# Kernel tuning notes

Hardware: AMD Instinct MI355X
Metric: run time of the kernel (lower is better)

The kernel has to match this reference:

```python
import jax, jax.numpy as jnp
import numpy as np
from functools import partial

L, B, E, H, NL = 512, 16, 768, 12, 12
D = E // H  # head dim = 64
FF = 4 * E
LN_EPS = 1e-5


def gelu_new(x):
    # HF openai-gpt ACT_FNS['gelu'] (tanh approximation)
    c = np.sqrt(2.0 / np.pi).astype(np.float32)
    return 0.5 * x * (1.0 + jnp.tanh(c * (x + 0.044715 * x * x * x)))


def layer_norm(x, g, b):
    mu = jnp.mean(x, axis=-1, keepdims=True)
    var = jnp.mean(jnp.square(x - mu), axis=-1, keepdims=True)
    return (x - mu) * jax.lax.rsqrt(var + LN_EPS) * g + b


def setup_inputs() -> dict:
    key = jax.random.key(0)
    ks = jax.random.split(key, 8)
    s = 0.02
    x = jax.random.normal(ks[0], (L, B, E), dtype=jnp.float32)
    custom_mask = jnp.ones((B, L), dtype=jnp.float32)
    pos_emb = s * jax.random.normal(ks[1], (L, E), dtype=jnp.float32)
    # stacked per-layer params (leading axis = layer)
    params = {
        'c_attn_w': s * jax.random.normal(ks[2], (NL, E, 3 * E), dtype=jnp.float32),
        'c_attn_b': jnp.zeros((NL, 3 * E), dtype=jnp.float32),
        'attn_proj_w': s * jax.random.normal(ks[3], (NL, E, E), dtype=jnp.float32),
        'attn_proj_b': jnp.zeros((NL, E), dtype=jnp.float32),
        'ln1_g': jnp.ones((NL, E), dtype=jnp.float32),
        'ln1_b': jnp.zeros((NL, E), dtype=jnp.float32),
        'c_fc_w': s * jax.random.normal(ks[4], (NL, E, FF), dtype=jnp.float32),
        'c_fc_b': jnp.zeros((NL, FF), dtype=jnp.float32),
        'mlp_proj_w': s * jax.random.normal(ks[5], (NL, FF, E), dtype=jnp.float32),
        'mlp_proj_b': jnp.zeros((NL, E), dtype=jnp.float32),
        'ln2_g': jnp.ones((NL, E), dtype=jnp.float32),
        'ln2_b': jnp.zeros((NL, E), dtype=jnp.float32),
    }
    return {'x': x, 'custom_mask': custom_mask, 'pos_emb': pos_emb, **params}


def _gpt_forward(x, custom_mask, pos_emb, c_attn_w, c_attn_b, attn_proj_w,
                 attn_proj_b, ln1_g, ln1_b, c_fc_w, c_fc_b, mlp_proj_w,
                 mlp_proj_b, ln2_g, ln2_b):
    Lx, Bx, Ex = x.shape
    h = x.transpose(1, 0, 2) + pos_emb[None, :Lx]  # (B, L, E); dropout = eval identity
    # additive padding mask: (1 - m) * finfo.min, broadcast over heads/queries
    add_mask = (1.0 - custom_mask)[:, None, None, :] * jnp.finfo(jnp.float32).min
    causal = jnp.tril(jnp.ones((Lx, Lx), dtype=jnp.float32))  # bias buffer b

    def block(h, p):
        (caw, cab, apw, apb, g1, b1, fw, fb, pw, pb, g2, b2) = p
        qkv = h @ caw + cab                              # (B, L, 3E)
        q, k, v = jnp.split(qkv, 3, axis=-1)
        q = q.reshape(Bx, Lx, H, D).transpose(0, 2, 1, 3)  # (B, H, L, D)
        k = k.reshape(Bx, Lx, H, D).transpose(0, 2, 1, 3)
        v = v.reshape(Bx, Lx, H, D).transpose(0, 2, 1, 3)
        w = jnp.einsum('bhqd,bhkd->bhqk', q, k) / np.float32(np.sqrt(D))
        w = w * causal + (-10000.0) * (1.0 - causal)     # causal bias masking
        w = w + add_mask
        a = jax.nn.softmax(w, axis=-1)
        o = jnp.einsum('bhqk,bhkd->bhqd', a, v)          # (B, H, L, D)
        o = o.transpose(0, 2, 1, 3).reshape(Bx, Lx, Ex)
        a_out = o @ apw + apb
        n = layer_norm(h + a_out, g1, b1)
        m = gelu_new(n @ fw + fb) @ pw + pb
        h2 = layer_norm(n + m, g2, b2)
        return h2, None

    params = (c_attn_w, c_attn_b, attn_proj_w, attn_proj_b, ln1_g, ln1_b,
              c_fc_w, c_fc_b, mlp_proj_w, mlp_proj_b, ln2_g, ln2_b)
    h, _ = jax.lax.scan(block, h, params)
    return h.transpose(1, 0, 2)  # back to (L, B, E)


def reference(x, custom_mask, pos_emb, c_attn_w, c_attn_b, attn_proj_w,
              attn_proj_b, ln1_g, ln1_b, c_fc_w, c_fc_b, mlp_proj_w,
              mlp_proj_b, ln2_g, ln2_b):
    return _gpt_forward(x, custom_mask, pos_emb, c_attn_w, c_attn_b,
                        attn_proj_w, attn_proj_b, ln1_g, ln1_b, c_fc_w,
                        c_fc_b, mlp_proj_w, mlp_proj_b, ln2_g, ln2_b)
```

## Files before the change

### kernel.cpp

```cpp
#include <hip/hip_runtime.h>
#include <cstdint>
#include <cstddef>


#define LSEQ 512
#define NBATCH 16
#define EDIM 768
#define NHEAD 12
#define NLAYER 12

typedef __attribute__((ext_vector_type(8))) short short8;
typedef __attribute__((ext_vector_type(4))) short short4v;
typedef __attribute__((ext_vector_type(4))) float f32x4;

__device__ __forceinline__ short f2bf(float f) {
  union { float f; unsigned u; } x; x.f = f;
  return (short)((x.u + 0x7FFFu + ((x.u >> 16) & 1u)) >> 16);
}
__device__ __forceinline__ float bf2f(short s) {
  union { unsigned u; float f; } x; x.u = ((unsigned)(unsigned short)s) << 16;
  return x.f;
}

__device__ __forceinline__ void gload_lds16(const void* g, void* l) {
  __builtin_amdgcn_global_load_lds(
      (__attribute__((address_space(1))) void*)(void*)g,
      (__attribute__((address_space(3))) void*)l, 16, 0, 0);
}

__global__ __launch_bounds__(256) void wt_transpose(const float* __restrict__ W,
                                                    short* __restrict__ Wt,
                                                    int K, int N) {
  __shared__ float tile[32][33];
  const int n0 = blockIdx.x * 32, k0 = blockIdx.y * 32;
  const size_t lo = (size_t)blockIdx.z * K * N;
  const float* Ws = W + lo;
  short* Wd = Wt + lo;
  const int tx = threadIdx.x & 31, ty = threadIdx.x >> 5;
#pragma unroll
  for (int i = 0; i < 4; ++i)
    tile[ty + i * 8][tx] = Ws[(size_t)(k0 + ty + i * 8) * N + n0 + tx];
  __syncthreads();
#pragma unroll
  for (int i = 0; i < 4; ++i)
    Wd[(size_t)(n0 + ty + i * 8) * K + k0 + tx] = f2bf(tile[tx][ty + i * 8]);
}

__global__ __launch_bounds__(256) void embed_k(const float* __restrict__ x,
                                               const float* __restrict__ pos,
                                               float* __restrict__ h,
                                               short* __restrict__ hbf) {
  const int row = blockIdx.x;
  const int b = row >> 9, lp = row & 511;
  const int t = threadIdx.x;
#pragma unroll
  for (int i = 0; i < 3; ++i) {
    const int e = t + i * 256;
    float v = x[(size_t)(lp * 16 + b) * 768 + e] + pos[(size_t)lp * 768 + e];
    h[(size_t)row * 768 + e] = v;
    hbf[(size_t)row * 768 + e] = f2bf(v);
  }
}

__global__ __launch_bounds__(256) void final_k(const float* __restrict__ h,
                                               float* __restrict__ out) {
  const int row = blockIdx.x;
  const int lp = row >> 4, b = row & 15;
  const int t = threadIdx.x;
#pragma unroll
  for (int i = 0; i < 3; ++i) {
    const int e = t + i * 256;
    out[(size_t)row * 768 + e] = h[(size_t)(b * 512 + lp) * 768 + e];
  }
}

__global__ __launch_bounds__(256) void ln_fused(const float* __restrict__ A,
                                                const short* __restrict__ B0,
                                                const short* __restrict__ B1,
                                                const float* __restrict__ g,
                                                const float* __restrict__ be,
                                                float* __restrict__ outf,
                                                short* __restrict__ outb) {
  const int row = blockIdx.x * 4 + (threadIdx.x >> 6);
  const int l = threadIdx.x & 63;
  const size_t base = (size_t)row * 768;
  float v[12];
  float s1 = 0.f, s2 = 0.f;
#pragma unroll
  for (int j = 0; j < 3; ++j) {
    const int e = j * 256 + l * 4;
    f32x4 a = *(const f32x4*)&A[base + e];
    short4v b0 = *(const short4v*)&B0[base + e];
    short4v b1 = *(const short4v*)&B1[base + e];
#pragma unroll
    for (int q = 0; q < 4; ++q) {
      float x = a[q] + bf2f(b0[q]) + bf2f(b1[q]);
      v[j * 4 + q] = x; s1 += x; s2 += x * x;
    }
  }
#pragma unroll
  for (int m = 1; m < 64; m <<= 1) {
    s1 += __shfl_xor(s1, m);
    s2 += __shfl_xor(s2, m);
  }
  const float mu = s1 * (1.f / 768.f);
  const float rs = rsqrtf(s2 * (1.f / 768.f) - mu * mu + 1e-5f);
#pragma unroll
  for (int j = 0; j < 3; ++j) {
    const int e = j * 256 + l * 4;
    f32x4 gv = *(const f32x4*)&g[e];
    f32x4 bv = *(const f32x4*)&be[e];
    f32x4 of; short4v ob;
#pragma unroll
    for (int q = 0; q < 4; ++q) {
      float o = (v[j * 4 + q] - mu) * rs * gv[q] + bv[q];
      of[q] = o; ob[q] = f2bf(o);
    }
    *(f32x4*)&outf[base + e] = of;
    *(short4v*)&outb[base + e] = ob;
  }
}

template <int EPI>
__global__ __launch_bounds__(512) void gemm512(const short* __restrict__ A,
                                               const short* __restrict__ Bt,
                                               const float* __restrict__ bias,
                                               short* __restrict__ C,
                                               int N, int K) {
  constexpr int BK = 64;
  __shared__ alignas(16) short Alds[128 * BK];
  __shared__ alignas(16) short Blds[256 * BK];
  const int t = threadIdx.x;
  const int w = t >> 6, l = t & 63;
  const int wr = w >> 2, wc = w & 3;
  const int l15 = l & 15, lhi = l >> 4;
  const int rowA0 = blockIdx.x * 128;
  const int rowB0 = blockIdx.y * 256;

  f32x4 acc[4][4];
#pragma unroll
  for (int mi = 0; mi < 4; ++mi)
#pragma unroll
    for (int ni = 0; ni < 4; ++ni) acc[mi][ni] = (f32x4){0.f, 0.f, 0.f, 0.f};

  const int srl = w * 8 + (l >> 3);
  const int ss = l & 7;

  const short* aptr[2];
#pragma unroll
  for (int i = 0; i < 2; ++i) {
    const int r = i * 64 + srl;
    aptr[i] = A + (size_t)(rowA0 + r) * K + ((ss ^ (r & 7)) << 3);
  }
  const short* bptr[4];
#pragma unroll
  for (int i = 0; i < 4; ++i) {
    const int r = i * 64 + srl;
    bptr[i] = Bt + (size_t)(rowB0 + r) * K + ((ss ^ (r & 7)) << 3);
  }

  for (int kt = 0; kt < K; kt += BK) {
#pragma unroll
    for (int i = 0; i < 2; ++i) {
      gload_lds16(aptr[i], &Alds[(i * 64 + w * 8) * BK]);
      aptr[i] += BK;
    }
#pragma unroll
    for (int i = 0; i < 4; ++i) {
      gload_lds16(bptr[i], &Blds[(i * 64 + w * 8) * BK]);
      bptr[i] += BK;
    }
    __syncthreads();
    short8 af[4][2], bfr[4][2];
#pragma unroll
    for (int mi = 0; mi < 4; ++mi) {
      const int r = wr * 64 + mi * 16 + l15;
#pragma unroll
      for (int kc = 0; kc < 2; ++kc)
        af[mi][kc] = *(const short8*)
            &Alds[r * BK + ((((kc << 2) | lhi) ^ (r & 7)) << 3)];
    }
#pragma unroll
    for (int ni = 0; ni < 4; ++ni) {
      const int r = wc * 64 + ni * 16 + l15;
#pragma unroll
      for (int kc = 0; kc < 2; ++kc)
        bfr[ni][kc] = *(const short8*)
            &Blds[r * BK + ((((kc << 2) | lhi) ^ (r & 7)) << 3)];
    }
#pragma unroll
    for (int mi = 0; mi < 4; ++mi)
#pragma unroll
      for (int ni = 0; ni < 4; ++ni)
#pragma unroll
        for (int kc = 0; kc < 2; ++kc)
          acc[mi][ni] = __builtin_amdgcn_mfma_f32_16x16x32_bf16(
              af[mi][kc], bfr[ni][kc], acc[mi][ni], 0, 0, 0);
    __syncthreads();
  }

  float bv[4];
#pragma unroll
  for (int ni = 0; ni < 4; ++ni) bv[ni] = bias[rowB0 + wc * 64 + ni * 16 + l15];
#pragma unroll
  for (int mi = 0; mi < 4; ++mi) {
#pragma unroll
    for (int ni = 0; ni < 4; ++ni) {
      const int col = rowB0 + wc * 64 + ni * 16 + l15;
#pragma unroll
      for (int i = 0; i < 4; ++i) {
        const int row = rowA0 + wr * 64 + mi * 16 + lhi * 4 + i;
        float v = acc[mi][ni][i] + bv[ni];
        if constexpr (EPI == 1) {
          C[(size_t)row * N + col] = f2bf(v);
        } else {
          float pz = v * fmaf(0.044715f, v * v, 1.0f);
          float e = __expf(-1.5957691216057308f * pz);
          float r = __builtin_amdgcn_rcpf(1.0f + e);
          C[(size_t)row * N + col] = f2bf(v * r);
        }
      }
    }
  }
}

__global__ __launch_bounds__(256) void gemm_pk(const short* __restrict__ A,
                                               const short* __restrict__ Bt,
                                               const float* __restrict__ bias,
                                               short* __restrict__ C,
                                               int N, int Kfull) {
  constexpr int BK = 64;
  __shared__ alignas(16) short Alds[128 * BK];
  __shared__ alignas(16) short Blds[128 * BK];
  const int t = threadIdx.x;
  const int w = t >> 6, l = t & 63;
  const int wr = w >> 1, wc = w & 1;
  const int l15 = l & 15, lhi = l >> 4;
  const int rowA0 = blockIdx.x * 128;
  const int rowB0 = blockIdx.y * 128;
  const int z = blockIdx.z;
  const int Ks = Kfull >> 1;
  const int koff = z * Ks;
  short* Cp = C + (size_t)z * 8192 * N;

  f32x4 acc[4][4];
#pragma unroll
  for (int mi = 0; mi < 4; ++mi)
#pragma unroll
    for (int ni = 0; ni < 4; ++ni) acc[mi][ni] = (f32x4){0.f, 0.f, 0.f, 0.f};

  const int srl = l >> 3;
  const int ss = l & 7;

  const short* aptr[4];
  const short* bptr[4];
#pragma unroll
  for (int i = 0; i < 4; ++i) {
    const int r = i * 32 + w * 8 + srl;
    aptr[i] = A + (size_t)(rowA0 + r) * Kfull + koff + ((ss ^ (r & 7)) << 3);
    bptr[i] = Bt + (size_t)(rowB0 + r) * Kfull + koff + ((ss ^ (r & 7)) << 3);
  }

  for (int kt = 0; kt < Ks; kt += BK) {
#pragma unroll
    for (int i = 0; i < 4; ++i) {
      gload_lds16(aptr[i], &Alds[i * 2048 + w * 512]);
      gload_lds16(bptr[i], &Blds[i * 2048 + w * 512]);
      aptr[i] += BK; bptr[i] += BK;
    }
    __syncthreads();
    short8 af[4][2], bfr[4][2];
#pragma unroll
    for (int mi = 0; mi < 4; ++mi) {
      const int r = wr * 64 + mi * 16 + l15;
#pragma unroll
      for (int kc = 0; kc < 2; ++kc)
        af[mi][kc] = *(const short8*)
            &Alds[r * 64 + ((((kc << 2) | lhi) ^ (r & 7)) << 3)];
    }
#pragma unroll
    for (int ni = 0; ni < 4; ++ni) {
      const int r = wc * 64 + ni * 16 + l15;
#pragma unroll
      for (int kc = 0; kc < 2; ++kc)
        bfr[ni][kc] = *(const short8*)
            &Blds[r * 64 + ((((kc << 2) | lhi) ^ (r & 7)) << 3)];
    }
#pragma unroll
    for (int mi = 0; mi < 4; ++mi)
#pragma unroll
      for (int ni = 0; ni < 4; ++ni)
#pragma unroll
        for (int kc = 0; kc < 2; ++kc)
          acc[mi][ni] = __builtin_amdgcn_mfma_f32_16x16x32_bf16(
              af[mi][kc], bfr[ni][kc], acc[mi][ni], 0, 0, 0);
    __syncthreads();
  }

  float bv[4];
#pragma unroll
  for (int ni = 0; ni < 4; ++ni)
    bv[ni] = (z == 0) ? bias[rowB0 + wc * 64 + ni * 16 + l15] : 0.f;
#pragma unroll
  for (int mi = 0; mi < 4; ++mi) {
#pragma unroll
    for (int ni = 0; ni < 4; ++ni) {
      const int col = rowB0 + wc * 64 + ni * 16 + l15;
#pragma unroll
      for (int i = 0; i < 4; ++i) {
        const int row = rowA0 + wr * 64 + mi * 16 + lhi * 4 + i;
        Cp[(size_t)row * N + col] = f2bf(acc[mi][ni][i] + bv[ni]);
      }
    }
  }
}

__global__ __launch_bounds__(256) void attn_k(const short* __restrict__ qkv,
                                              const float* __restrict__ mask,
                                              short* __restrict__ o) {
  const int qb = blockIdx.x;
  const int hh = blockIdx.y;
  const int b = blockIdx.z;
  const int t = threadIdx.x, w = t >> 6, l = t & 63;
  const int l15 = l & 15, lhi = l >> 4;
  __shared__ alignas(16) short Klds[64 * 64];
  __shared__ alignas(16) short Vlds[64 * 64];
  __shared__ alignas(16) short Plds[4][16 * 72];

  short8 qa[2];
  {
    const size_t base =
        (size_t)(b * LSEQ + qb * 64 + w * 16 + l15) * 2304 + hh * 64;
    qa[0] = *(const short8*)&qkv[base + lhi * 8];
    qa[1] = *(const short8*)&qkv[base + 32 + lhi * 8];
  }
  float mrow[4] = {-1e30f, -1e30f, -1e30f, -1e30f};
  float lrow[4] = {0.f, 0.f, 0.f, 0.f};
  const f32x4 zero4 = {0.f, 0.f, 0.f, 0.f};
  f32x4 oacc[4];
#pragma unroll
  for (int nt = 0; nt < 4; ++nt) oacc[nt] = zero4;

  const int nkt = qb + 1;
  for (int kt = 0; kt < nkt; ++kt) {
    __syncthreads();
    {
      const int kr = t >> 2, cc = (t & 3) * 16;
      const size_t grow = (size_t)(b * LSEQ + kt * 64 + kr) * 2304 + hh * 64;
      short8 k0 = *(const short8*)&qkv[grow + 768 + cc];
      short8 k1 = *(const short8*)&qkv[grow + 768 + cc + 8];
      short8 v0 = *(const short8*)&qkv[grow + 1536 + cc];
      short8 v1 = *(const short8*)&qkv[grow + 1536 + cc + 8];
      const int sw = (kr & 7) << 4;
      *(short8*)((char*)Klds + ((kr * 128 + cc * 2) ^ sw)) = k0;
      *(short8*)((char*)Klds + ((kr * 128 + cc * 2 + 16) ^ sw)) = k1;
#pragma unroll
      for (int e = 0; e < 8; ++e) {
        const int n0 = cc + e, n1 = cc + 8 + e;
        ((short*)Vlds)[((n0 * 128 + kr * 2) ^ ((n0 & 7) << 4)) >> 1] = v0[e];
        ((short*)Vlds)[((n1 * 128 + kr * 2) ^ ((n1 & 7) << 4)) >> 1] = v1[e];
      }
    }
    __syncthreads();

    f32x4 s[4];
#pragma unroll
    for (int jt = 0; jt < 4; ++jt) {
      f32x4 z = zero4;
#pragma unroll
      for (int kc = 0; kc < 2; ++kc) {
        const int rowk = jt * 16 + l15;
        short8 kb = *(const short8*)((char*)Klds +
                     ((rowk * 128 + kc * 64 + lhi * 16) ^ ((rowk & 7) << 4)));
        z = __builtin_amdgcn_mfma_f32_16x16x32_bf16(qa[kc], kb, z, 0, 0, 0);
      }
      s[jt] = z;
    }

    float addm[4];
#pragma unroll
    for (int jt = 0; jt < 4; ++jt)
      addm[jt] = (1.0f - mask[b * LSEQ + kt * 64 + jt * 16 + l15]) *
                 -3.402823466e38f;
#pragma unroll
    for (int jt = 0; jt < 4; ++jt) {
      const int colg = kt * 64 + jt * 16 + l15;
#pragma unroll
      for (int i = 0; i < 4; ++i) {
        const int rowg = qb * 64 + w * 16 + lhi * 4 + i;
        float sv = s[jt][i] * 0.125f;
        if (colg > rowg) sv = -10000.0f;
        s[jt][i] = sv + addm[jt];
      }
    }

    float mnew[4], sc[4];
#pragma unroll
    for (int i = 0; i < 4; ++i) {
      float tm = fmaxf(fmaxf(s[0][i], s[1][i]), fmaxf(s[2][i], s[3][i]));
#pragma unroll
      for (int mm = 1; mm < 16; mm <<= 1) tm = fmaxf(tm, __shfl_xor(tm, mm));
      mnew[i] = fmaxf(mrow[i], tm);
      sc[i] = __expf(mrow[i] - mnew[i]);
      mrow[i] = mnew[i];
    }
#pragma unroll
    for (int i = 0; i < 4; ++i) {
      float ts = 0.f;
#pragma unroll
      for (int jt = 0; jt < 4; ++jt) {
        float p = __expf(s[jt][i] - mnew[i]);
        s[jt][i] = p;
        ts += p;
      }
#pragma unroll
      for (int mm = 1; mm < 16; mm <<= 1) ts += __shfl_xor(ts, mm);
      lrow[i] = lrow[i] * sc[i] + ts;
      oacc[0][i] *= sc[i]; oacc[1][i] *= sc[i];
      oacc[2][i] *= sc[i]; oacc[3][i] *= sc[i];
    }

    short* Pw = &Plds[w][0];
#pragma unroll
    for (int jt = 0; jt < 4; ++jt)
#pragma unroll
      for (int i = 0; i < 4; ++i)
        Pw[(lhi * 4 + i) * 72 + jt * 16 + l15] = f2bf(s[jt][i]);
    __syncthreads();
    short8 pa[2];
#pragma unroll
    for (int kc = 0; kc < 2; ++kc)
      pa[kc] = *(const short8*)&Pw[l15 * 72 + kc * 32 + lhi * 8];

#pragma unroll
    for (int nt = 0; nt < 4; ++nt) {
#pragma unroll
      for (int kc = 0; kc < 2; ++kc) {
        const int rown = nt * 16 + l15;
        short8 vb = *(const short8*)((char*)Vlds +
                     ((rown * 128 + kc * 64 + lhi * 16) ^ ((rown & 7) << 4)));
        oacc[nt] = __builtin_amdgcn_mfma_f32_16x16x32_bf16(pa[kc], vb,
                                                           oacc[nt], 0, 0, 0);
      }
    }
  }

#pragma unroll
  for (int i = 0; i < 4; ++i) {
    const size_t row = (size_t)(b * LSEQ + qb * 64 + w * 16 + lhi * 4 + i);
    const float inv = 1.0f / lrow[i];
#pragma unroll
    for (int nt = 0; nt < 4; ++nt)
      o[row * 768 + hh * 64 + nt * 16 + l15] = f2bf(oacc[nt][i] * inv);
  }
}

extern "C" void kernel_launch(void* const* d_in, const int* in_sizes, int n_in,
                              void* d_out, int out_size, void* d_ws,
                              size_t ws_size, hipStream_t stream) {
  const float* x    = (const float*)d_in[0];
  const float* mask = (const float*)d_in[1];
  const float* pos  = (const float*)d_in[2];
  const float* caw  = (const float*)d_in[3];
  const float* cab  = (const float*)d_in[4];
  const float* apw  = (const float*)d_in[5];
  const float* apb  = (const float*)d_in[6];
  const float* g1   = (const float*)d_in[7];
  const float* b1   = (const float*)d_in[8];
  const float* fw   = (const float*)d_in[9];
  const float* fb   = (const float*)d_in[10];
  const float* pw   = (const float*)d_in[11];
  const float* pb   = (const float*)d_in[12];
  const float* g2   = (const float*)d_in[13];
  const float* b2   = (const float*)d_in[14];

  char* ws = (char*)d_ws;
  size_t off = 0;
  auto alloc = [&](size_t bytes) {
    size_t o = off;
    off += (bytes + 255) & ~(size_t)255;
    return o;
  };
  float* h    = (float*)(ws + alloc(8192ull * 768 * 4));
  short* hbf  = (short*)(ws + alloc(8192ull * 768 * 2));
  float* nrm  = (float*)(ws + alloc(8192ull * 768 * 4));
  short* nbf  = (short*)(ws + alloc(8192ull * 768 * 2));
  short* qkvb = (short*)(ws + alloc(8192ull * 2304 * 2));
  short* obf  = (short*)(ws + alloc(8192ull * 768 * 2));
  short* aout = (short*)(ws + alloc(2ull * 8192 * 768 * 2));
  short* gbf  = (short*)(ws + alloc(8192ull * 3072 * 2));
  short* wt_attn = (short*)(ws + alloc(12ull * 768 * 2304 * 2));
  short* wt_proj = (short*)(ws + alloc(12ull * 768 * 768 * 2));
  short* wt_fc   = (short*)(ws + alloc(12ull * 768 * 3072 * 2));
  short* wt_mlp  = (short*)(ws + alloc(12ull * 3072 * 768 * 2));
  short* aout1 = aout + 8192ull * 768;
  (void)ws_size; (void)in_sizes; (void)n_in; (void)out_size;

  wt_transpose<<<dim3(2304 / 32, 768 / 32, 12), 256, 0, stream>>>(caw, wt_attn, 768, 2304);
  wt_transpose<<<dim3(768 / 32, 768 / 32, 12), 256, 0, stream>>>(apw, wt_proj, 768, 768);
  wt_transpose<<<dim3(3072 / 32, 768 / 32, 12), 256, 0, stream>>>(fw, wt_fc, 768, 3072);
  wt_transpose<<<dim3(768 / 32, 3072 / 32, 12), 256, 0, stream>>>(pw, wt_mlp, 3072, 768);

  embed_k<<<8192, 256, 0, stream>>>(x, pos, h, hbf);

  for (int L = 0; L < 12; ++L) {
    gemm512<1><<<dim3(64, 9), 512, 0, stream>>>(
        hbf, wt_attn + (size_t)L * 2304 * 768, cab + (size_t)L * 2304, qkvb, 2304, 768);
    attn_k<<<dim3(8, 12, 16), 256, 0, stream>>>(qkvb, mask, obf);
    gemm_pk<<<dim3(64, 6, 2), 256, 0, stream>>>(
        obf, wt_proj + (size_t)L * 768 * 768, apb + (size_t)L * 768, aout, 768, 768);
    ln_fused<<<2048, 256, 0, stream>>>(h, aout, aout1, g1 + (size_t)L * 768,
                                       b1 + (size_t)L * 768, nrm, nbf);
    gemm512<2><<<dim3(64, 12), 512, 0, stream>>>(
        nbf, wt_fc + (size_t)L * 768 * 3072, fb + (size_t)L * 3072, gbf, 3072, 768);
    gemm_pk<<<dim3(64, 6, 2), 256, 0, stream>>>(
        gbf, wt_mlp + (size_t)L * 3072 * 768, pb + (size_t)L * 768, aout, 768, 3072);
    ln_fused<<<2048, 256, 0, stream>>>(nrm, aout, aout1, g2 + (size_t)L * 768,
                                       b2 + (size_t)L * 768, h, hbf);
  }

  final_k<<<8192, 256, 0, stream>>>(h, (float*)d_out);
}
```

Before: 3.265 ms.

## Shrink QKV/FC GEMM tiles to 64x256 with 256 threads; fuse final transpose into LN

The QKV and FC GEMMs move from 128x256 tiles with 512 threads (8 waves) to 64x256 tiles with 256 threads (4 waves). This doubles the grid size, which is meant to improve CU occupancy and load balance, at the cost of loading the B tile twice as often per output. Separately, the last layer's LayerNorm now writes directly into the output in (L,B,E) order, which removes the final_k copy kernel and the unused bf16 store.

```diff
diff --git a/kernel.cpp b/kernel.cpp
--- a/kernel.cpp
+++ b/kernel.cpp
@@ -62,18 +62,7 @@
   }
 }
 
-__global__ __launch_bounds__(256) void final_k(const float* __restrict__ h,
-                                               float* __restrict__ out) {
-  const int row = blockIdx.x;
-  const int lp = row >> 4, b = row & 15;
-  const int t = threadIdx.x;
-#pragma unroll
-  for (int i = 0; i < 3; ++i) {
-    const int e = t + i * 256;
-    out[(size_t)row * 768 + e] = h[(size_t)(b * 512 + lp) * 768 + e];
-  }
-}
-
+template <int FINAL>
 __global__ __launch_bounds__(256) void ln_fused(const float* __restrict__ A,
                                                 const short* __restrict__ B0,
                                                 const short* __restrict__ B1,
@@ -105,6 +94,11 @@
   }
   const float mu = s1 * (1.f / 768.f);
   const float rs = rsqrtf(s2 * (1.f / 768.f) - mu * mu + 1e-5f);
+  size_t obase = base;
+  if constexpr (FINAL) {
+    const int b = row >> 9, lp = row & 511;
+    obase = (size_t)(lp * 16 + b) * 768;
+  }
 #pragma unroll
   for (int j = 0; j < 3; ++j) {
     const int e = j * 256 + l * 4;
@@ -116,25 +110,25 @@
       float o = (v[j * 4 + q] - mu) * rs * gv[q] + bv[q];
       of[q] = o; ob[q] = f2bf(o);
     }
-    *(f32x4*)&outf[base + e] = of;
-    *(short4v*)&outb[base + e] = ob;
+    *(f32x4*)&outf[obase + e] = of;
+    if constexpr (!FINAL) *(short4v*)&outb[obase + e] = ob;
   }
 }
 
 template <int EPI>
-__global__ __launch_bounds__(512) void gemm512(const short* __restrict__ A,
+__global__ __launch_bounds__(256) void gemm256(const short* __restrict__ A,
                                                const short* __restrict__ Bt,
                                                const float* __restrict__ bias,
                                                short* __restrict__ C,
                                                int N, int K) {
   constexpr int BK = 64;
-  __shared__ alignas(16) short Alds[128 * BK];
+  __shared__ alignas(16) short Alds[64 * BK];
   __shared__ alignas(16) short Blds[256 * BK];
   const int t = threadIdx.x;
   const int w = t >> 6, l = t & 63;
-  const int wr = w >> 2, wc = w & 3;
+  const int wc = w;
   const int l15 = l & 15, lhi = l >> 4;
-  const int rowA0 = blockIdx.x * 128;
+  const int rowA0 = blockIdx.x * 64;
   const int rowB0 = blockIdx.y * 256;
 
   f32x4 acc[4][4];
@@ -149,32 +143,32 @@
   const short* aptr[2];
 #pragma unroll
   for (int i = 0; i < 2; ++i) {
-    const int r = i * 64 + srl;
+    const int r = i * 32 + srl;
     aptr[i] = A + (size_t)(rowA0 + r) * K + ((ss ^ (r & 7)) << 3);
   }
-  const short* bptr[4];
-#pragma unroll
-  for (int i = 0; i < 4; ++i) {
-    const int r = i * 64 + srl;
+  const short* bptr[8];
+#pragma unroll
+  for (int i = 0; i < 8; ++i) {
+    const int r = i * 32 + srl;
     bptr[i] = Bt + (size_t)(rowB0 + r) * K + ((ss ^ (r & 7)) << 3);
   }
 
   for (int kt = 0; kt < K; kt += BK) {
 #pragma unroll
     for (int i = 0; i < 2; ++i) {
-      gload_lds16(aptr[i], &Alds[(i * 64 + w * 8) * BK]);
+      gload_lds16(aptr[i], &Alds[(i * 32 + w * 8) * BK]);
       aptr[i] += BK;
     }
 #pragma unroll
-    for (int i = 0; i < 4; ++i) {
-      gload_lds16(bptr[i], &Blds[(i * 64 + w * 8) * BK]);
+    for (int i = 0; i < 8; ++i) {
+      gload_lds16(bptr[i], &Blds[(i * 32 + w * 8) * BK]);
       bptr[i] += BK;
     }
     __syncthreads();
     short8 af[4][2], bfr[4][2];
 #pragma unroll
     for (int mi = 0; mi < 4; ++mi) {
-      const int r = wr * 64 + mi * 16 + l15;
+      const int r = mi * 16 + l15;
 #pragma unroll
       for (int kc = 0; kc < 2; ++kc)
         af[mi][kc] = *(const short8*)
@@ -209,7 +203,7 @@
       const int col = rowB0 + wc * 64 + ni * 16 + l15;
 #pragma unroll
       for (int i = 0; i < 4; ++i) {
-        const int row = rowA0 + wr * 64 + mi * 16 + lhi * 4 + i;
+        const int row = rowA0 + mi * 16 + lhi * 4 + i;
         float v = acc[mi][ni][i] + bv[ni];
         if constexpr (EPI == 1) {
           C[(size_t)row * N + col] = f2bf(v);
@@ -504,20 +498,24 @@
   embed_k<<<8192, 256, 0, stream>>>(x, pos, h, hbf);
 
   for (int L = 0; L < 12; ++L) {
-    gemm512<1><<<dim3(64, 9), 512, 0, stream>>>(
+    gemm256<1><<<dim3(128, 9), 256, 0, stream>>>(
         hbf, wt_attn + (size_t)L * 2304 * 768, cab + (size_t)L * 2304, qkvb, 2304, 768);
     attn_k<<<dim3(8, 12, 16), 256, 0, stream>>>(qkvb, mask, obf);
     gemm_pk<<<dim3(64, 6, 2), 256, 0, stream>>>(
         obf, wt_proj + (size_t)L * 768 * 768, apb + (size_t)L * 768, aout, 768, 768);
-    ln_fused<<<2048, 256, 0, stream>>>(h, aout, aout1, g1 + (size_t)L * 768,
-                                       b1 + (size_t)L * 768, nrm, nbf);
-    gemm512<2><<<dim3(64, 12), 512, 0, stream>>>(
+    ln_fused<0><<<2048, 256, 0, stream>>>(h, aout, aout1, g1 + (size_t)L * 768,
+                                          b1 + (size_t)L * 768, nrm, nbf);
+    gemm256<2><<<dim3(128, 12), 256, 0, stream>>>(
         nbf, wt_fc + (size_t)L * 768 * 3072, fb + (size_t)L * 3072, gbf, 3072, 768);
     gemm_pk<<<dim3(64, 6, 2), 256, 0, stream>>>(
         gbf, wt_mlp + (size_t)L * 3072 * 768, pb + (size_t)L * 768, aout, 768, 3072);
-    ln_fused<<<2048, 256, 0, stream>>>(nrm, aout, aout1, g2 + (size_t)L * 768,
-                                       b2 + (size_t)L * 768, h, hbf);
-  }
-
-  final_k<<<8192, 256, 0, stream>>>(h, (float*)d_out);
-}
+    if (L < 11) {
+      ln_fused<0><<<2048, 256, 0, stream>>>(nrm, aout, aout1, g2 + (size_t)L * 768,
+                                            b2 + (size_t)L * 768, h, hbf);
+    } else {
+      ln_fused<1><<<2048, 256, 0, stream>>>(nrm, aout, aout1, g2 + (size_t)L * 768,
+                                            b2 + (size_t)L * 768, (float*)d_out,
+                                            nullptr);
+    }
+  }
+}
```

Result: no change. 3.247 ms (-0.6%).

## Pre-transpose V, use direct LDS loads in attention, drop fp32 residual stream

Applied to the files above, without the earlier changes.

Adds a V transpose kernel after the QKV GEMM so attention can load K and transposed V tiles with direct global-to-LDS 16-byte loads, replacing the per-element scattered LDS transpose writes. The residual stream is kept only in bf16: the fp32 h and nrm buffers are removed and layer norm reads the bf16 copy. The final layer norm writes the output directly in the (L,B,E) layout, removing the final copy kernel. The cost is an extra kernel launch and V round-trip per layer, and a loss of residual precision from carrying it in bf16.

```diff
diff --git a/kernel.cpp b/kernel.cpp
--- a/kernel.cpp
+++ b/kernel.cpp
@@ -46,9 +46,32 @@
     Wd[(size_t)(n0 + ty + i * 8) * K + k0 + tx] = f2bf(tile[tx][ty + i * 8]);
 }
 
+__global__ __launch_bounds__(256) void v_transpose(const short* __restrict__ qkv,
+                                                   short* __restrict__ Vt) {
+  __shared__ short tile[64][72];
+  const int m0 = blockIdx.x * 64;
+  const int d0 = blockIdx.y * 64;
+  const int t = threadIdx.x;
+  const int tx = t & 7, ty = t >> 3;
+#pragma unroll
+  for (int i = 0; i < 2; ++i) {
+    const int m = ty + i * 32;
+    *(short8*)&tile[m][tx * 8] =
+        *(const short8*)&qkv[(size_t)(m0 + m) * 2304 + 1536 + d0 + tx * 8];
+  }
+  __syncthreads();
+#pragma unroll
+  for (int i = 0; i < 2; ++i) {
+    const int d = ty + i * 32;
+    short8 vv;
+#pragma unroll
+    for (int j = 0; j < 8; ++j) vv[j] = tile[tx * 8 + j][d];
+    *(short8*)&Vt[(size_t)(d0 + d) * 8192 + m0 + tx * 8] = vv;
+  }
+}
+
 __global__ __launch_bounds__(256) void embed_k(const float* __restrict__ x,
                                                const float* __restrict__ pos,
-                                               float* __restrict__ h,
                                                short* __restrict__ hbf) {
   const int row = blockIdx.x;
   const int b = row >> 9, lp = row & 511;
@@ -57,30 +80,17 @@
   for (int i = 0; i < 3; ++i) {
     const int e = t + i * 256;
     float v = x[(size_t)(lp * 16 + b) * 768 + e] + pos[(size_t)lp * 768 + e];
-    h[(size_t)row * 768 + e] = v;
     hbf[(size_t)row * 768 + e] = f2bf(v);
   }
 }
 
-__global__ __launch_bounds__(256) void final_k(const float* __restrict__ h,
-                                               float* __restrict__ out) {
-  const int row = blockIdx.x;
-  const int lp = row >> 4, b = row & 15;
-  const int t = threadIdx.x;
-#pragma unroll
-  for (int i = 0; i < 3; ++i) {
-    const int e = t + i * 256;
-    out[(size_t)row * 768 + e] = h[(size_t)(b * 512 + lp) * 768 + e];
-  }
-}
-
-__global__ __launch_bounds__(256) void ln_fused(const float* __restrict__ A,
+template <int FINAL>
+__global__ __launch_bounds__(256) void ln_fused(const short* __restrict__ A,
                                                 const short* __restrict__ B0,
                                                 const short* __restrict__ B1,
                                                 const float* __restrict__ g,
                                                 const float* __restrict__ be,
-                                                float* __restrict__ outf,
-                                                short* __restrict__ outb) {
+                                                void* __restrict__ out) {
   const int row = blockIdx.x * 4 + (threadIdx.x >> 6);
   const int l = threadIdx.x & 63;
   const size_t base = (size_t)row * 768;
@@ -89,12 +99,12 @@
 #pragma unroll
   for (int j = 0; j < 3; ++j) {
     const int e = j * 256 + l * 4;
-    f32x4 a = *(const f32x4*)&A[base + e];
+    short4v a = *(const short4v*)&A[base + e];
     short4v b0 = *(const short4v*)&B0[base + e];
     short4v b1 = *(const short4v*)&B1[base + e];
 #pragma unroll
     for (int q = 0; q < 4; ++q) {
-      float x = a[q] + bf2f(b0[q]) + bf2f(b1[q]);
+      float x = bf2f(a[q]) + bf2f(b0[q]) + bf2f(b1[q]);
       v[j * 4 + q] = x; s1 += x; s2 += x * x;
     }
   }
@@ -105,19 +115,29 @@
   }
   const float mu = s1 * (1.f / 768.f);
   const float rs = rsqrtf(s2 * (1.f / 768.f) - mu * mu + 1e-5f);
+  size_t obase = base;
+  if constexpr (FINAL) {
+    const int b = row >> 9, lp = row & 511;
+    obase = (size_t)(lp * 16 + b) * 768;
+  }
 #pragma unroll
   for (int j = 0; j < 3; ++j) {
     const int e = j * 256 + l * 4;
     f32x4 gv = *(const f32x4*)&g[e];
     f32x4 bv = *(const f32x4*)&be[e];
-    f32x4 of; short4v ob;
-#pragma unroll
-    for (int q = 0; q < 4; ++q) {
-      float o = (v[j * 4 + q] - mu) * rs * gv[q] + bv[q];
-      of[q] = o; ob[q] = f2bf(o);
-    }
-    *(f32x4*)&outf[base + e] = of;
-    *(short4v*)&outb[base + e] = ob;
+    if constexpr (FINAL) {
+      f32x4 of;
+#pragma unroll
+      for (int q = 0; q < 4; ++q)
+        of[q] = (v[j * 4 + q] - mu) * rs * gv[q] + bv[q];
+      *(f32x4*)&((float*)out)[obase + e] = of;
+    } else {
+      short4v ob;
+#pragma unroll
+      for (int q = 0; q < 4; ++q)
+        ob[q] = f2bf((v[j * 4 + q] - mu) * rs * gv[q] + bv[q]);
+      *(short4v*)&((short*)out)[obase + e] = ob;
+    }
   }
 }
 
@@ -316,6 +336,7 @@
 }
 
 __global__ __launch_bounds__(256) void attn_k(const short* __restrict__ qkv,
+                                              const short* __restrict__ Vt,
                                               const float* __restrict__ mask,
                                               short* __restrict__ o) {
   const int qb = blockIdx.x;
@@ -325,7 +346,6 @@
   const int l15 = l & 15, lhi = l >> 4;
   __shared__ alignas(16) short Klds[64 * 64];
   __shared__ alignas(16) short Vlds[64 * 64];
-  __shared__ alignas(16) short Plds[4][16 * 72];
 
   short8 qa[2];
   {
@@ -334,6 +354,7 @@
     qa[0] = *(const short8*)&qkv[base + lhi * 8];
     qa[1] = *(const short8*)&qkv[base + 32 + lhi * 8];
   }
+  __shared__ alignas(16) short Plds[4][16 * 72];
   float mrow[4] = {-1e30f, -1e30f, -1e30f, -1e30f};
   float lrow[4] = {0.f, 0.f, 0.f, 0.f};
   const f32x4 zero4 = {0.f, 0.f, 0.f, 0.f};
@@ -341,25 +362,19 @@
 #pragma unroll
   for (int nt = 0; nt < 4; ++nt) oacc[nt] = zero4;
 
+  const int lr = l >> 3, sl = l & 7;
   const int nkt = qb + 1;
   for (int kt = 0; kt < nkt; ++kt) {
     __syncthreads();
-    {
-      const int kr = t >> 2, cc = (t & 3) * 16;
-      const size_t grow = (size_t)(b * LSEQ + kt * 64 + kr) * 2304 + hh * 64;
-      short8 k0 = *(const short8*)&qkv[grow + 768 + cc];
-      short8 k1 = *(const short8*)&qkv[grow + 768 + cc + 8];
-      short8 v0 = *(const short8*)&qkv[grow + 1536 + cc];
-      short8 v1 = *(const short8*)&qkv[grow + 1536 + cc + 8];
-      const int sw = (kr & 7) << 4;
-      *(short8*)((char*)Klds + ((kr * 128 + cc * 2) ^ sw)) = k0;
-      *(short8*)((char*)Klds + ((kr * 128 + cc * 2 + 16) ^ sw)) = k1;
-#pragma unroll
-      for (int e = 0; e < 8; ++e) {
-        const int n0 = cc + e, n1 = cc + 8 + e;
-        ((short*)Vlds)[((n0 * 128 + kr * 2) ^ ((n0 & 7) << 4)) >> 1] = v0[e];
-        ((short*)Vlds)[((n1 * 128 + kr * 2) ^ ((n1 & 7) << 4)) >> 1] = v1[e];
-      }
+#pragma unroll
+    for (int i = 0; i < 2; ++i) {
+      const int kr = i * 32 + w * 8 + lr;
+      gload_lds16(qkv + (size_t)(b * LSEQ + kt * 64 + kr) * 2304 + 768 +
+                      hh * 64 + ((sl ^ (kr & 7)) << 3),
+                  &Klds[(i * 32 + w * 8) * 64]);
+      gload_lds16(Vt + (size_t)(hh * 64 + kr) * 8192 + b * LSEQ + kt * 64 +
+                      ((sl ^ (kr & 7)) << 3),
+                  &Vlds[(i * 32 + w * 8) * 64]);
     }
     __syncthreads();
 
@@ -481,11 +496,10 @@
     off += (bytes + 255) & ~(size_t)255;
     return o;
   };
-  float* h    = (float*)(ws + alloc(8192ull * 768 * 4));
   short* hbf  = (short*)(ws + alloc(8192ull * 768 * 2));
-  float* nrm  = (float*)(ws + alloc(8192ull * 768 * 4));
   short* nbf  = (short*)(ws + alloc(8192ull * 768 * 2));
   short* qkvb = (short*)(ws + alloc(8192ull * 2304 * 2));
+  short* vT   = (short*)(ws + alloc(768ull * 8192 * 2));
   short* obf  = (short*)(ws + alloc(8192ull * 768 * 2));
   short* aout = (short*)(ws + alloc(2ull * 8192 * 768 * 2));
   short* gbf  = (short*)(ws + alloc(8192ull * 3072 * 2));
@@ -501,23 +515,27 @@
   wt_transpose<<<dim3(3072 / 32, 768 / 32, 12), 256, 0, stream>>>(fw, wt_fc, 768, 3072);
   wt_transpose<<<dim3(768 / 32, 3072 / 32, 12), 256, 0, stream>>>(pw, wt_mlp, 3072, 768);
 
-  embed_k<<<8192, 256, 0, stream>>>(x, pos, h, hbf);
+  embed_k<<<8192, 256, 0, stream>>>(x, pos, hbf);
 
   for (int L = 0; L < 12; ++L) {
     gemm512<1><<<dim3(64, 9), 512, 0, stream>>>(
         hbf, wt_attn + (size_t)L * 2304 * 768, cab + (size_t)L * 2304, qkvb, 2304, 768);
-    attn_k<<<dim3(8, 12, 16), 256, 0, stream>>>(qkvb, mask, obf);
+    v_transpose<<<dim3(128, 12), 256, 0, stream>>>(qkvb, vT);
+    attn_k<<<dim3(8, 12, 16), 256, 0, stream>>>(qkvb, vT, mask, obf);
     gemm_pk<<<dim3(64, 6, 2), 256, 0, stream>>>(
         obf, wt_proj + (size_t)L * 768 * 768, apb + (size_t)L * 768, aout, 768, 768);
-    ln_fused<<<2048, 256, 0, stream>>>(h, aout, aout1, g1 + (size_t)L * 768,
-                                       b1 + (size_t)L * 768, nrm, nbf);
+    ln_fused<0><<<2048, 256, 0, stream>>>(hbf, aout, aout1, g1 + (size_t)L * 768,
+                                          b1 + (size_t)L * 768, nbf);
     gemm512<2><<<dim3(64, 12), 512, 0, stream>>>(
         nbf, wt_fc + (size_t)L * 768 * 3072, fb + (size_t)L * 3072, gbf, 3072, 768);
     gemm_pk<<<dim3(64, 6, 2), 256, 0, stream>>>(
         gbf, wt_mlp + (size_t)L * 3072 * 768, pb + (size_t)L * 768, aout, 768, 3072);
-    ln_fused<<<2048, 256, 0, stream>>>(nrm, aout, aout1, g2 + (size_t)L * 768,
-                                       b2 + (size_t)L * 768, h, hbf);
-  }
-
-  final_k<<<8192, 256, 0, stream>>>(h, (float*)d_out);
-}
+    if (L < 11) {
+      ln_fused<0><<<2048, 256, 0, stream>>>(nbf, aout, aout1, g2 + (size_t)L * 768,
+                                            b2 + (size_t)L * 768, hbf);
+    } else {
+      ln_fused<1><<<2048, 256, 0, stream>>>(nbf, aout, aout1, g2 + (size_t)L * 768,
+                                            b2 + (size_t)L * 768, (float*)d_out);
+    }
+  }
+}
```

New measurement: 3.147 ms. 3.6% less time.
